# Performance work log

Hardware: AMD Instinct MI355X
Metric: run time of the kernel (lower is better)

The kernel has to match this reference:

```python
import jax, jax.numpy as jnp
import numpy as np

N = 50000          # nodes
E = 1600000        # edges (before self-loops)
IN = 512           # in_channels
H = 8              # heads
C1 = 8             # per-head channels of conv1 (== heads)
OUT = 64           # out_channels
SLOPE = 0.2        # GATConv leaky_relu negative slope


def setup_inputs() -> dict:
    key = jax.random.key(0)
    ks = jax.random.split(key, 10)
    x = jax.random.normal(ks[0], (N, IN), jnp.float32)
    edge_index = jax.random.randint(ks[1], (2, E), 0, N, dtype=jnp.int64)
    s1 = 1.0 / np.sqrt(IN)
    s2 = 1.0 / np.sqrt(H * C1)
    W1 = jax.random.normal(ks[2], (IN, H * C1), jnp.float32) * s1
    att_src1 = jax.random.normal(ks[3], (H, C1), jnp.float32) * s2
    att_dst1 = jax.random.normal(ks[4], (H, C1), jnp.float32) * s2
    b1 = jnp.zeros((H * C1,), jnp.float32)
    W2 = jax.random.normal(ks[5], (H * C1, OUT), jnp.float32) * s2
    att_src2 = jax.random.normal(ks[6], (1, OUT), jnp.float32) * 0.1
    att_dst2 = jax.random.normal(ks[7], (1, OUT), jnp.float32) * 0.1
    b2 = jnp.zeros((OUT,), jnp.float32)
    return {"x": x, "edge_index": edge_index, "W1": W1, "att_src1": att_src1,
            "att_dst1": att_dst1, "b1": b1, "W2": W2, "att_src2": att_src2,
            "att_dst2": att_dst2, "b2": b2}


def gat_layer(x, src, dst, W, a_src, a_dst, b, heads, ch, concat):
    n = x.shape[0]
    h = (x @ W).reshape(n, heads, ch)                       # [N,H,C]
    alpha_src = jnp.einsum('nhc,hc->nh', h, a_src)          # [N,H]
    alpha_dst = jnp.einsum('nhc,hc->nh', h, a_dst)
    e = jax.nn.leaky_relu(alpha_src[src] + alpha_dst[dst], SLOPE)  # [Etot,H]
    # segment softmax over incoming edges of each destination node
    m = jax.ops.segment_max(e, dst, num_segments=n)
    ex = jnp.exp(e - m[dst])
    denom = jax.ops.segment_sum(ex, dst, num_segments=n)
    alpha = ex / (denom[dst] + 1e-16)                       # [Etot,H]
    out = jax.ops.segment_sum(h[src] * alpha[:, :, None], dst, num_segments=n)
    out = out.reshape(n, heads * ch) if concat else out.mean(axis=1)
    return out + b


def reference(x, edge_index, W1, att_src1, att_dst1, b1, W2, att_src2, att_dst2, b2):
    n = x.shape[0]
    loops = jnp.arange(n, dtype=edge_index.dtype)           # add_self_loops=True
    src = jnp.concatenate([edge_index[0], loops])
    dst = jnp.concatenate([edge_index[1], loops])
    h = jax.nn.elu(gat_layer(x, src, dst, W1, att_src1, att_dst1, b1, H, C1, True))
    # F.dropout in eval mode is identity
    out = gat_layer(h, src, dst, W2, att_src2, att_dst2, b2, 1, OUT, False)
    return jax.nn.log_softmax(out, axis=-1)
```

## Files before the change

### kernel.cpp

```cpp
#include <hip/hip_runtime.h>
#include <hip/hip_bf16.h>
#include <math.h>


#define WAVE 64
#define NPB_SHIFT 7
#define NB_MAX 512
#define NBLK 128
#define CAP 6144

typedef __attribute__((ext_vector_type(8))) short short8;
typedef __attribute__((ext_vector_type(4))) float f32x4;

__device__ inline float wred_sum(float v) {
#pragma unroll
    for (int off = 32; off > 0; off >>= 1) v += __shfl_xor(v, off);
    return v;
}
__device__ inline float wred_max(float v) {
#pragma unroll
    for (int off = 32; off > 0; off >>= 1) v = fmaxf(v, __shfl_xor(v, off));
    return v;
}
__device__ inline unsigned short f2bf(float f) {
    unsigned u = __float_as_uint(f);
    u += 0x7FFFu + ((u >> 16) & 1u);
    return (unsigned short)(u >> 16);
}
__device__ inline float bf2f(unsigned short u) {
    return __uint_as_float((unsigned)u << 16);
}

__global__ __launch_bounds__(256) void bucket_count(const int* __restrict__ ei,
                                                    int* __restrict__ hist,
                                                    int E, int Et, int NB, int epb) {
    __shared__ int lh[NB_MAX];
    for (int t = threadIdx.x; t < NB; t += 256) lh[t] = 0;
    __syncthreads();
    int e0 = blockIdx.x * epb;
    int e1 = min(e0 + epb, Et);
    for (int e = e0 + threadIdx.x; e < e1; e += 256) {
        int d = (e < E) ? ei[E + e] : (e - E);
        atomicAdd(&lh[d >> NPB_SHIFT], 1);
    }
    __syncthreads();
    for (int t = threadIdx.x; t < NB; t += 256)
        hist[blockIdx.x * NB + t] = lh[t];
}

__global__ __launch_bounds__(512) void bucket_scan(int* __restrict__ hist,
                                                   int* __restrict__ bBase,
                                                   int* __restrict__ rowptr,
                                                   int NB, int nblk, int n) {
    __shared__ int tot[NB_MAX];
    for (int b = threadIdx.x; b < NB; b += 512) {
        int s = 0;
        for (int j = 0; j < nblk; ++j) s += hist[j * NB + b];
        tot[b] = s;
    }
    __syncthreads();
    if (threadIdx.x == 0) {
        int run = 0;
        for (int b = 0; b < NB; ++b) { int t = tot[b]; tot[b] = run; bBase[b] = run; run += t; }
        bBase[NB] = run;
        rowptr[n] = run;
    }
    __syncthreads();
    for (int b = threadIdx.x; b < NB; b += 512) {
        int run = tot[b];
        for (int j = 0; j < nblk; ++j) { int t = hist[j * NB + b]; hist[j * NB + b] = run; run += t; }
    }
}

__global__ __launch_bounds__(256) void bucket_scatter(const int* __restrict__ ei,
                                                      const int* __restrict__ hist,
                                                      unsigned* __restrict__ region,
                                                      int E, int Et, int NB, int epb) {
    __shared__ int gb[NB_MAX];
    __shared__ int off[NB_MAX];
    for (int t = threadIdx.x; t < NB; t += 256) { gb[t] = hist[blockIdx.x * NB + t]; off[t] = 0; }
    __syncthreads();
    int e0 = blockIdx.x * epb;
    int e1 = min(e0 + epb, Et);
    for (int e = e0 + threadIdx.x; e < e1; e += 256) {
        int s, d;
        if (e < E) { s = ei[e]; d = ei[E + e]; }
        else       { s = d = e - E; }
        int b = d >> NPB_SHIFT;
        int p = gb[b] + atomicAdd(&off[b], 1);
        region[p] = (unsigned)s | ((unsigned)(d & 127) << 16);
    }
}

__global__ __launch_bounds__(256) void bucket_build(unsigned* __restrict__ region,
                                                    const int* __restrict__ bBase,
                                                    int* __restrict__ rowptr, int n) {
    __shared__ int deg[128], rp[129], cur[128];
    __shared__ unsigned short sb[CAP];
    int b = blockIdx.x;
    int base = bBase[b];
    int cnt  = min(bBase[b + 1] - base, CAP);
    int tid  = threadIdx.x;
    if (tid < 128) { deg[tid] = 0; cur[tid] = 0; }
    __syncthreads();
    for (int i = tid; i < cnt; i += 256)
        atomicAdd(&deg[region[base + i] >> 16], 1);
    __syncthreads();
    if (tid == 0) {
        int run = 0;
        for (int t = 0; t < 128; ++t) { rp[t] = run; run += deg[t]; }
        rp[128] = run;
    }
    __syncthreads();
    int nodeLo = b << NPB_SHIFT;
    if (tid < 128 && nodeLo + tid < n) rowptr[nodeLo + tid] = base + rp[tid];
    for (int i = tid; i < cnt; i += 256) {
        unsigned v = region[base + i];
        int dl = v >> 16;
        int p = rp[dl] + atomicAdd(&cur[dl], 1);
        sb[p] = (unsigned short)(v & 0xFFFFu);
    }
    __syncthreads();
    for (int i = tid; i < cnt; i += 256)
        region[base + i] = (unsigned)sb[i];
}

__global__ __launch_bounds__(256) void wtrans_kernel(const float* __restrict__ W,
                                                     unsigned short* __restrict__ wtg) {
    int idx = blockIdx.x * 256 + threadIdx.x;
    if (idx >= 64 * 512) return;
    int c = idx >> 9, k = idx & 511;
    wtg[c * 512 + k] = f2bf(W[k * 64 + c]);
}

__global__ __launch_bounds__(256) void wtrans2_kernel(const float* __restrict__ W,
                                                      unsigned short* __restrict__ wt2) {
    int idx = blockIdx.x * 256 + threadIdx.x;
    if (idx >= 64 * 64) return;
    int c = idx >> 6, k = idx & 63;
    wt2[c * 64 + k] = f2bf(W[k * 64 + c]);
}

__global__ __launch_bounds__(256) void gemm1_mfma(const float* __restrict__ X,
                                                  const unsigned short* __restrict__ wtg,
                                                  unsigned short* __restrict__ O, int nrows) {
    __shared__ unsigned short xs[64][40];
    __shared__ unsigned short wt[64][40];
    int tid  = threadIdx.x;
    int wid  = tid >> 6;
    int lane = tid & 63;
    int lr   = lane & 15;
    int lg   = lane >> 4;
    int bm   = blockIdx.x * 64;

    f32x4 acc[4];
#pragma unroll
    for (int i = 0; i < 4; ++i) acc[i] = (f32x4){0.f, 0.f, 0.f, 0.f};

    for (int k0 = 0; k0 < 512; k0 += 32) {
#pragma unroll
        for (int i = 0; i < 2; ++i) {
            int p = tid + i * 256;
            int row = p >> 3, c4 = p & 7;
            float4 v = {0.f, 0.f, 0.f, 0.f};
            if (bm + row < nrows)
                v = *(const float4*)(X + (size_t)(bm + row) * 512 + k0 + c4 * 4);
            unsigned short* dst = &xs[row][c4 * 4];
            dst[0] = f2bf(v.x); dst[1] = f2bf(v.y); dst[2] = f2bf(v.z); dst[3] = f2bf(v.w);
        }
        {
            int c = tid >> 2, kq = tid & 3;
            *(short8*)&wt[c][kq * 8] = *(const short8*)&wtg[c * 512 + k0 + kq * 8];
        }
        __syncthreads();
        short8 af = *(short8*)&xs[wid * 16 + lr][lg * 8];
#pragma unroll
        for (int cb = 0; cb < 4; ++cb) {
            short8 bfb = *(short8*)&wt[cb * 16 + lr][lg * 8];
            acc[cb] = __builtin_amdgcn_mfma_f32_16x16x32_bf16(af, bfb, acc[cb], 0, 0, 0);
        }
        __syncthreads();
    }
#pragma unroll
    for (int cb = 0; cb < 4; ++cb)
#pragma unroll
        for (int r = 0; r < 4; ++r) {
            int m = bm + wid * 16 + lg * 4 + r;
            if (m < nrows) O[(size_t)m * 64 + cb * 16 + lr] = f2bf(acc[cb][r]);
        }
}

__global__ __launch_bounds__(256) void gemm2_mfma(const unsigned short* __restrict__ X,
                                                  const unsigned short* __restrict__ wt2,
                                                  unsigned short* __restrict__ O, int nrows) {
    __shared__ unsigned short xs[64][40];
    __shared__ unsigned short wt[64][40];
    int tid  = threadIdx.x;
    int wid  = tid >> 6;
    int lane = tid & 63;
    int lr   = lane & 15;
    int lg   = lane >> 4;
    int bm   = blockIdx.x * 64;

    f32x4 acc[4];
#pragma unroll
    for (int i = 0; i < 4; ++i) acc[i] = (f32x4){0.f, 0.f, 0.f, 0.f};

#pragma unroll
    for (int k0 = 0; k0 < 64; k0 += 32) {
        {
            int row = tid >> 2, kq = tid & 3;
            short8 v = {0, 0, 0, 0, 0, 0, 0, 0};
            if (bm + row < nrows)
                v = *(const short8*)&X[(size_t)(bm + row) * 64 + k0 + kq * 8];
            *(short8*)&xs[row][kq * 8] = v;
        }
        {
            int c = tid >> 2, kq = tid & 3;
            *(short8*)&wt[c][kq * 8] = *(const short8*)&wt2[c * 64 + k0 + kq * 8];
        }
        __syncthreads();
        short8 af = *(short8*)&xs[wid * 16 + lr][lg * 8];
#pragma unroll
        for (int cb = 0; cb < 4; ++cb) {
            short8 bfb = *(short8*)&wt[cb * 16 + lr][lg * 8];
            acc[cb] = __builtin_amdgcn_mfma_f32_16x16x32_bf16(af, bfb, acc[cb], 0, 0, 0);
        }
        __syncthreads();
    }
#pragma unroll
    for (int cb = 0; cb < 4; ++cb)
#pragma unroll
        for (int r = 0; r < 4; ++r) {
            int m = bm + wid * 16 + lg * 4 + r;
            if (m < nrows) O[(size_t)m * 64 + cb * 16 + lr] = f2bf(acc[cb][r]);
        }
}

__global__ __launch_bounds__(256) void alpha1_kernel(const unsigned short* __restrict__ H1b,
                                                     const float* __restrict__ as1,
                                                     const float* __restrict__ ad1,
                                                     unsigned short* __restrict__ asrc,
                                                     float* __restrict__ adst, int n) {
    int idx = blockIdx.x * 256 + threadIdx.x;
    if (idx >= n * 8) return;
    int h = idx & 7;
    const unsigned short* hp = H1b + (size_t)(idx >> 3) * 64 + h * 8;
    short8 hv = *(const short8*)hp;
    float s = 0.f, d = 0.f;
#pragma unroll
    for (int c = 0; c < 8; ++c) {
        float v = bf2f((unsigned short)hv[c]);
        s = fmaf(v, as1[h * 8 + c], s);
        d = fmaf(v, ad1[h * 8 + c], d);
    }
    asrc[idx] = f2bf(s);
    adst[idx] = d;
}

__global__ __launch_bounds__(256) void alpha2_kernel(const unsigned short* __restrict__ H2b,
                                                     const float* __restrict__ as2,
                                                     const float* __restrict__ ad2,
                                                     float* __restrict__ asrc,
                                                     float* __restrict__ adst, int n) {
    int node = blockIdx.x * 4 + (threadIdx.x >> 6);
    int lane = threadIdx.x & 63;
    if (node >= n) return;
    float v = bf2f(H2b[(size_t)node * 64 + lane]);
    float s = wred_sum(v * as2[lane]);
    float d = wred_sum(v * ad2[lane]);
    if (lane == 0) { asrc[node] = s; adst[node] = d; }
}

__global__ __launch_bounds__(256) void agg1_kernel(const unsigned short* __restrict__ H1b,
                                                   const unsigned short* __restrict__ asrc,
                                                   const float* __restrict__ adst,
                                                   const int* __restrict__ rowptr,
                                                   const int* __restrict__ csrc,
                                                   const float* __restrict__ b1,
                                                   unsigned short* __restrict__ out1, int n) {
    __shared__ float wbuf[4][64][8];
    __shared__ int   sbuf[4][64];
    int wid  = threadIdx.x >> 6;
    int lane = threadIdx.x & 63;
    int node = blockIdx.x * 4 + wid;
    if (node >= n) return;
    int h = lane >> 3;
    int beg = rowptr[node], end = rowptr[node + 1];

    float ad[8];
    *(float4*)&ad[0] = *(const float4*)&adst[(size_t)node * 8];
    *(float4*)&ad[4] = *(const float4*)&adst[(size_t)node * 8 + 4];

    float lsum[8];
#pragma unroll
    for (int i = 0; i < 8; ++i) lsum[i] = 0.f;
    float acc0 = 0.f, acc1 = 0.f;

    for (int c0 = beg; c0 < end; c0 += 64) {
        int e = c0 + lane;
        if (e < end) {
            int s = csrc[e];
            sbuf[wid][lane] = s;
            short8 av = *(const short8*)&asrc[(size_t)s * 8];
            float p[8];
#pragma unroll
            for (int i = 0; i < 8; ++i) {
                float t = bf2f((unsigned short)av[i]) + ad[i];
                t = t > 0.f ? t : 0.2f * t;
                p[i] = __expf(t);
                lsum[i] += p[i];
            }
            *(float4*)&wbuf[wid][lane][0] = *(float4*)&p[0];
            *(float4*)&wbuf[wid][lane][4] = *(float4*)&p[4];
        }
        int cnt = min(64, end - c0);
        int i = 0;
        for (; i + 3 < cnt; i += 4) {
            int s0 = sbuf[wid][i + 0], s1 = sbuf[wid][i + 1];
            int s2 = sbuf[wid][i + 2], s3 = sbuf[wid][i + 3];
            float w0 = wbuf[wid][i + 0][h], w1 = wbuf[wid][i + 1][h];
            float w2 = wbuf[wid][i + 2][h], w3 = wbuf[wid][i + 3][h];
            float g0 = bf2f(H1b[(size_t)s0 * 64 + lane]);
            float g1 = bf2f(H1b[(size_t)s1 * 64 + lane]);
            float g2 = bf2f(H1b[(size_t)s2 * 64 + lane]);
            float g3 = bf2f(H1b[(size_t)s3 * 64 + lane]);
            acc0 = fmaf(g0, w0, acc0);
            acc1 = fmaf(g1, w1, acc1);
            acc0 = fmaf(g2, w2, acc0);
            acc1 = fmaf(g3, w3, acc1);
        }
        for (; i < cnt; ++i) {
            int s   = sbuf[wid][i];
            float w = wbuf[wid][i][h];
            acc0 = fmaf(bf2f(H1b[(size_t)s * 64 + lane]), w, acc0);
        }
    }
    float acc = acc0 + acc1;
#pragma unroll
    for (int off = 32; off > 0; off >>= 1)
#pragma unroll
        for (int i = 0; i < 8; ++i) lsum[i] += __shfl_xor(lsum[i], off);
    float L = lsum[0];
#pragma unroll
    for (int i = 1; i < 8; ++i) if (h == i) L = lsum[i];
    float o = acc / (L + 1e-16f) + b1[lane];
    o = o > 0.f ? o : expm1f(o);
    out1[(size_t)node * 64 + lane] = f2bf(o);
}

__global__ __launch_bounds__(256) void agg2_kernel(const unsigned short* __restrict__ H2b,
                                                   const float* __restrict__ asrc,
                                                   const float* __restrict__ adst,
                                                   const int* __restrict__ rowptr,
                                                   const int* __restrict__ csrc,
                                                   const float* __restrict__ b2,
                                                   float* __restrict__ out, int n) {
    __shared__ float wbuf[4][64];
    __shared__ int   sbuf[4][64];
    int wid  = threadIdx.x >> 6;
    int lane = threadIdx.x & 63;
    int node = blockIdx.x * 4 + wid;
    if (node >= n) return;
    int beg = rowptr[node], end = rowptr[node + 1];
    float ad = adst[node];

    float lsum = 0.f, acc0 = 0.f, acc1 = 0.f;
    for (int c0 = beg; c0 < end; c0 += 64) {
        int e = c0 + lane;
        if (e < end) {
            int s = csrc[e];
            sbuf[wid][lane] = s;
            float t = asrc[s] + ad;
            t = t > 0.f ? t : 0.2f * t;
            float p = __expf(t);
            lsum += p;
            wbuf[wid][lane] = p;
        }
        int cnt = min(64, end - c0);
        int i = 0;
        for (; i + 3 < cnt; i += 4) {
            int s0 = sbuf[wid][i + 0], s1 = sbuf[wid][i + 1];
            int s2 = sbuf[wid][i + 2], s3 = sbuf[wid][i + 3];
            float w0 = wbuf[wid][i + 0], w1 = wbuf[wid][i + 1];
            float w2 = wbuf[wid][i + 2], w3 = wbuf[wid][i + 3];
            float g0 = bf2f(H2b[(size_t)s0 * 64 + lane]);
            float g1 = bf2f(H2b[(size_t)s1 * 64 + lane]);
            float g2 = bf2f(H2b[(size_t)s2 * 64 + lane]);
            float g3 = bf2f(H2b[(size_t)s3 * 64 + lane]);
            acc0 = fmaf(g0, w0, acc0);
            acc1 = fmaf(g1, w1, acc1);
            acc0 = fmaf(g2, w2, acc0);
            acc1 = fmaf(g3, w3, acc1);
        }
        for (; i < cnt; ++i) {
            acc0 = fmaf(bf2f(H2b[(size_t)sbuf[wid][i] * 64 + lane]), wbuf[wid][i], acc0);
        }
    }
    lsum = wred_sum(lsum);
    float o = (acc0 + acc1) / (lsum + 1e-16f) + b2[lane];
    float mx = wred_max(o);
    float se = wred_sum(__expf(o - mx));
    out[(size_t)node * 64 + lane] = o - mx - logf(se);
}

extern "C" void kernel_launch(void* const* d_in, const int* in_sizes, int n_in,
                              void* d_out, int out_size, void* d_ws, size_t ws_size,
                              hipStream_t stream) {
    const float* x   = (const float*)d_in[0];
    const int*   ei  = (const int*)d_in[1];
    const float* W1  = (const float*)d_in[2];
    const float* as1 = (const float*)d_in[3];
    const float* ad1 = (const float*)d_in[4];
    const float* b1  = (const float*)d_in[5];
    const float* W2  = (const float*)d_in[6];
    const float* as2 = (const float*)d_in[7];
    const float* ad2 = (const float*)d_in[8];
    const float* b2  = (const float*)d_in[9];
    float* out = (float*)d_out;

    const int n  = in_sizes[0] / 512;
    const int E  = in_sizes[1] / 2;
    const int Et = E + n;
    const int NB  = (n + 127) >> NPB_SHIFT;
    const int epb = (Et + NBLK - 1) / NBLK;

    char* w = (char*)d_ws;
    auto alloc = [&](size_t bytes) {
        char* p = w;
        w += (bytes + 255) & ~(size_t)255;
        return p;
    };
    int*            hist   = (int*)alloc((size_t)NBLK * NB * 4);
    int*            bBase  = (int*)alloc((size_t)(NB + 1) * 4);
    unsigned*       region = (unsigned*)alloc((size_t)Et * 4);
    int*            rowptr = (int*)alloc((size_t)(n + 1) * 4);
    unsigned short* h1b    = (unsigned short*)alloc((size_t)n * 64 * 2);
    unsigned short* out1b  = (unsigned short*)alloc((size_t)n * 64 * 2);
    unsigned short* h2b    = (unsigned short*)alloc((size_t)n * 64 * 2);
    unsigned short* asrc1b = (unsigned short*)alloc((size_t)n * 8 * 2);
    float*          adst1  = (float*)alloc((size_t)n * 8 * 4);
    float*          asrc2  = (float*)alloc((size_t)n * 4);
    float*          adst2  = (float*)alloc((size_t)n * 4);
    unsigned short* wtg    = (unsigned short*)alloc((size_t)64 * 512 * 2);
    unsigned short* wtg2   = (unsigned short*)alloc((size_t)64 * 64 * 2);
    int*            csrc   = (int*)region;

    bucket_count  <<<NBLK, 256, 0, stream>>>(ei, hist, E, Et, NB, epb);
    bucket_scan   <<<1,    512, 0, stream>>>(hist, bBase, rowptr, NB, NBLK, n);
    bucket_scatter<<<NBLK, 256, 0, stream>>>(ei, hist, region, E, Et, NB, epb);
    bucket_build  <<<NB,   256, 0, stream>>>(region, bBase, rowptr, n);

    wtrans_kernel<<<(64 * 512 + 255) / 256, 256, 0, stream>>>(W1, wtg);
    gemm1_mfma<<<(n + 63) / 64, 256, 0, stream>>>(x, wtg, h1b, n);
    alpha1_kernel<<<(n * 8 + 255) / 256, 256, 0, stream>>>(h1b, as1, ad1, asrc1b, adst1, n);
    agg1_kernel<<<(n + 3) / 4, 256, 0, stream>>>(h1b, asrc1b, adst1, rowptr, csrc, b1, out1b, n);

    wtrans2_kernel<<<(64 * 64 + 255) / 256, 256, 0, stream>>>(W2, wtg2);
    gemm2_mfma<<<(n + 63) / 64, 256, 0, stream>>>(out1b, wtg2, h2b, n);
    alpha2_kernel<<<(n + 3) / 4, 256, 0, stream>>>(h2b, as2, ad2, asrc2, adst2, n);
    agg2_kernel<<<(n + 3) / 4, 256, 0, stream>>>(h2b, asrc2, adst2, rowptr, csrc, b2, out, n);
}
```

Baseline: 415.1 us.

## Stage full W1 tile in LDS once and load X fragments directly to registers

The first-layer GEMM now loads the whole 64x512 bf16 weight matrix into shared memory once per block, with padding. Each lane reads its own X row fragments straight from global memory into MFMA operand registers. This removes the per-k-step X staging through LDS and the two barriers per iteration, and the fully unrolled k loop lets loads be issued early. In exchange it uses about 66KB of LDS per block, which may reduce occupancy, and each lane's X reads cover only 32 bytes per row.

Result: no change. 416.3 us (+0.3%).

```diff
diff --git a/kernel.cpp b/kernel.cpp
--- a/kernel.cpp
+++ b/kernel.cpp
@@ -144,8 +144,7 @@
 __global__ __launch_bounds__(256) void gemm1_mfma(const float* __restrict__ X,
                                                   const unsigned short* __restrict__ wtg,
                                                   unsigned short* __restrict__ O, int nrows) {
-    __shared__ unsigned short xs[64][40];
-    __shared__ unsigned short wt[64][40];
+    __shared__ unsigned short wt[64][520];
     int tid  = threadIdx.x;
     int wid  = tid >> 6;
     int lane = tid & 63;
@@ -153,33 +152,38 @@
     int lg   = lane >> 4;
     int bm   = blockIdx.x * 64;
 
+#pragma unroll
+    for (int i = 0; i < 16; ++i) {
+        int p  = tid + i * 256;
+        int r  = p >> 6, c8 = p & 63;
+        *(short8*)&wt[r][c8 * 8] = *(const short8*)&wtg[r * 512 + c8 * 8];
+    }
+    __syncthreads();
+
+    int arow  = bm + wid * 16 + lr;
+    bool valid = (arow < nrows);
+    const float* xrow = X + (size_t)arow * 512;
+
     f32x4 acc[4];
 #pragma unroll
     for (int i = 0; i < 4; ++i) acc[i] = (f32x4){0.f, 0.f, 0.f, 0.f};
 
-    for (int k0 = 0; k0 < 512; k0 += 32) {
-#pragma unroll
-        for (int i = 0; i < 2; ++i) {
-            int p = tid + i * 256;
-            int row = p >> 3, c4 = p & 7;
-            float4 v = {0.f, 0.f, 0.f, 0.f};
-            if (bm + row < nrows)
-                v = *(const float4*)(X + (size_t)(bm + row) * 512 + k0 + c4 * 4);
-            unsigned short* dst = &xs[row][c4 * 4];
-            dst[0] = f2bf(v.x); dst[1] = f2bf(v.y); dst[2] = f2bf(v.z); dst[3] = f2bf(v.w);
-        }
-        {
-            int c = tid >> 2, kq = tid & 3;
-            *(short8*)&wt[c][kq * 8] = *(const short8*)&wtg[c * 512 + k0 + kq * 8];
-        }
-        __syncthreads();
-        short8 af = *(short8*)&xs[wid * 16 + lr][lg * 8];
+#pragma unroll
+    for (int ks = 0; ks < 16; ++ks) {
+        int k0 = ks * 32 + lg * 8;
+        float4 v0 = {0.f, 0.f, 0.f, 0.f}, v1 = {0.f, 0.f, 0.f, 0.f};
+        if (valid) {
+            v0 = *(const float4*)(xrow + k0);
+            v1 = *(const float4*)(xrow + k0 + 4);
+        }
+        short8 af;
+        af[0] = f2bf(v0.x); af[1] = f2bf(v0.y); af[2] = f2bf(v0.z); af[3] = f2bf(v0.w);
+        af[4] = f2bf(v1.x); af[5] = f2bf(v1.y); af[6] = f2bf(v1.z); af[7] = f2bf(v1.w);
 #pragma unroll
         for (int cb = 0; cb < 4; ++cb) {
-            short8 bfb = *(short8*)&wt[cb * 16 + lr][lg * 8];
+            short8 bfb = *(short8*)&wt[cb * 16 + lr][ks * 32 + lg * 8];
             acc[cb] = __builtin_amdgcn_mfma_f32_16x16x32_bf16(af, bfb, acc[cb], 0, 0, 0);
         }
-        __syncthreads();
     }
 #pragma unroll
     for (int cb = 0; cb < 4; ++cb)
```
